# Performance work log

Hardware: AMD Instinct MI355X
Metric: run time of the kernel (lower is better)

## Reference

```python
import jax, jax.numpy as jnp
import numpy as np

B, N, D = 32, 2048, 128
NUM_QUERIES = 16
K_FRAC = 0.5
NUM_SUPPORTS = N - NUM_QUERIES
K_KEEP = int(K_FRAC * NUM_SUPPORTS)  # 1016
M = K_KEEP + NUM_QUERIES             # pooled node count, 1032


def setup_inputs() -> dict:
    key = jax.random.key(0)
    k1, k2, k3 = jax.random.split(key, 3)
    A = jax.random.normal(k1, (B, N, N), dtype=jnp.float32)
    X = jax.random.normal(k2, (B, N, D), dtype=jnp.float32)
    w = jax.random.normal(k3, (D,), dtype=jnp.float32) * 0.1  # proj weight (out_dim=1)
    b = jnp.zeros((1,), dtype=jnp.float32)                     # proj bias
    return {"A": A, "X": X, "w": w, "b": b}


def reference(A, X, w, b):
    # per-node scores: sigmoid(Linear(X)/100), shape [B, N]
    scores = jax.nn.sigmoid((jnp.einsum('bnd,d->bn', X, w) + b[0]) / 100.0)
    support_scores = scores[:, :NUM_SUPPORTS]                     # [B, S]
    intra = support_scores - support_scores.mean(axis=1, keepdims=True)
    # torch.topk(largest=False) == top_k of negated values (ascending order)
    _, support_idx = jax.lax.top_k(-intra, K_KEEP)                # [B, K]
    support_values = jnp.take_along_axis(support_scores, support_idx, axis=1)
    query_idx = jnp.broadcast_to(jnp.arange(NUM_SUPPORTS, N, dtype=support_idx.dtype), (B, NUM_QUERIES))
    query_values = scores[:, NUM_SUPPORTS:]
    idx = jnp.concatenate([support_idx, query_idx], axis=1)       # [B, M]
    values = jnp.concatenate([support_values, query_values], axis=1)  # [B, M]
    # gather + scale node features
    new_X = jnp.take_along_axis(X, idx[:, :, None], axis=1) * values[:, :, None]  # [B, M, D]
    # double gather on adjacency: A[i, idx][:, idx]
    rows = jnp.take_along_axis(A, idx[:, :, None], axis=1)        # [B, M, N]
    new_A = jnp.take_along_axis(rows, idx[:, None, :], axis=2)    # [B, M, M]
    return (new_A, new_X, idx)
```

## Files before the change

### kernel.cpp

```cpp
#include <hip/hip_runtime.h>

#define NB 32
#define NN 2048
#define ND 128
#define NSUP 2032
#define KKEEP 1016
#define MM 1032

typedef unsigned long long u64;
typedef unsigned int u32;

__device__ __forceinline__ float mulrn(float a, float b) {
  float r;
  asm("v_mul_f32 %0, %1, %2" : "=v"(r) : "v"(a), "v"(b));
  return r;
}
__device__ __forceinline__ float addrn(float a, float b) {
  float r;
  asm("v_add_f32 %0, %1, %2" : "=v"(r) : "v"(a), "v"(b));
  return r;
}
__device__ __forceinline__ float fmarn(float a, float b, float c) {
  float r;
  asm("v_fma_f32 %0, %1, %2, %3" : "=v"(r) : "v"(a), "v"(b), "v"(c));
  return r;
}

__global__ __launch_bounds__(256) void k_score(const float* __restrict__ X,
                                               const float* __restrict__ w,
                                               const float* __restrict__ bias,
                                               u64* __restrict__ keys,
                                               float* __restrict__ score) {
#pragma clang fp contract(off)
  int row = blockIdx.x * 256 + threadIdx.x;
  if (row >= NB * NN) return;
  const float* x = X + (size_t)row * ND;

  float l[16];
  #pragma unroll
  for (int k = 0; k < 16; ++k) l[k] = 0.f;
  #pragma unroll
  for (int step = 0; step < 8; ++step) {
    const float* xp = x + step * 16;
    const float* wp = w + step * 16;
    #pragma unroll
    for (int q4 = 0; q4 < 4; ++q4) {
      const float4 xv = *reinterpret_cast<const float4*>(xp + q4 * 4);
      const float4 wv = *reinterpret_cast<const float4*>(wp + q4 * 4);
      l[q4 * 4 + 0] = addrn(mulrn(xv.x, wv.x), l[q4 * 4 + 0]);
      l[q4 * 4 + 1] = addrn(mulrn(xv.y, wv.y), l[q4 * 4 + 1]);
      l[q4 * 4 + 2] = addrn(mulrn(xv.z, wv.z), l[q4 * 4 + 2]);
      l[q4 * 4 + 3] = addrn(mulrn(xv.w, wv.w), l[q4 * 4 + 3]);
    }
  }
  #pragma unroll
  for (int k = 0; k < 8; ++k) l[k] = addrn(l[k], l[k + 8]);
  #pragma unroll
  for (int k = 0; k < 4; ++k) l[k] = addrn(l[k], l[k + 4]);
  l[0] = addrn(l[0], l[2]);
  l[1] = addrn(l[1], l[3]);
  const float dot = addrn(l[0], l[1]);

  const float z = __fdiv_rn(addrn(dot, bias[0]), 100.0f);

  const float xe = -z;
  const float z2 = mulrn(xe, xe);
  float y = fmarn(1.9875691500E-4f, xe, 1.3981999507E-3f);
  y = fmarn(y, xe, 8.3334519073E-3f);
  y = fmarn(y, xe, 4.1665795894E-2f);
  y = fmarn(y, xe, 1.6666665459E-1f);
  y = fmarn(y, xe, 5.0000001201E-1f);
  y = fmarn(y, z2, xe);
  const float e = addrn(y, 1.0f);

  const float s = __fdiv_rn(1.0f, addrn(1.0f, e));

  score[row] = s;

  const u32 sb = __float_as_uint(s);
  const int n = row & (NN - 1);
  keys[row] = ((u64)sb << 32) | (u32)n;
}

__global__ __launch_bounds__(1024) void k_sort(const u64* __restrict__ keys,
                                               const float* __restrict__ score,
                                               int* __restrict__ idxs,
                                               float* __restrict__ vals,
                                               float* __restrict__ out_idx) {
  __shared__ u64 sk[NN];
  int b = blockIdx.x, t = threadIdx.x;
  for (int i = t; i < NN; i += 1024)
    sk[i] = (i < NSUP) ? keys[(size_t)b * NN + i] : ~0ull;
  __syncthreads();
  for (int k = 2; k <= NN; k <<= 1) {
    for (int j = k >> 1; j > 0; j >>= 1) {
      int i = ((t / j) * (j << 1)) + (t % j);
      int p = i + j;
      bool up = ((i & k) == 0);
      u64 ki = sk[i], kp = sk[p];
      if ((ki > kp) == up) { sk[i] = kp; sk[p] = ki; }
      __syncthreads();
    }
  }
  for (int i = t; i < MM; i += 1024) {
    int si = (i < KKEEP) ? (int)(sk[i] & 0xffffffffu) : (NSUP + (i - KKEEP));
    idxs[b * MM + i]    = si;
    vals[b * MM + i]    = score[(size_t)b * NN + si];
    out_idx[b * MM + i] = (float)si;
  }
}

__global__ __launch_bounds__(256) void k_newx(const float* __restrict__ X,
                                              const int* __restrict__ idxs,
                                              const float* __restrict__ vals,
                                              float* __restrict__ out_x) {
  int gid  = blockIdx.x * blockDim.x + threadIdx.x;
  int row  = gid >> 6;
  int lane = threadIdx.x & 63;
  if (row >= NB * MM) return;
  int b  = row / MM;
  int ri = idxs[row];
  float v = vals[row];
  const float2 x2 = *reinterpret_cast<const float2*>(X + ((size_t)b * NN + ri) * ND + lane * 2);
  float2 o = make_float2(x2.x * v, x2.y * v);
  *reinterpret_cast<float2*>(out_x + (size_t)row * ND + lane * 2) = o;
}

__global__ __launch_bounds__(256) void k_newa(const float* __restrict__ A,
                                              const int* __restrict__ idxs,
                                              float* __restrict__ out_a) {
  __shared__ float srow[NN];
  __shared__ int   scols[MM];
  int row = blockIdx.x;
  int b   = row / MM;
  const int* cols = idxs + b * MM;
  for (int i = threadIdx.x; i < MM; i += 256) scols[i] = cols[i];

  int ri = idxs[row];
  const float* arow = A + ((size_t)b * NN + ri) * NN;
  #pragma unroll
  for (int i = 0; i < 2; ++i) {
    int off = (threadIdx.x + i * 256) * 4;
    *reinterpret_cast<float4*>(&srow[off]) =
        *reinterpret_cast<const float4*>(arow + off);
  }
  __syncthreads();

  float4* orow = reinterpret_cast<float4*>(out_a + (size_t)row * MM);
  for (int c = threadIdx.x; c < MM / 4; c += 256) {
    const int4 j4 = *reinterpret_cast<const int4*>(scols + c * 4);
    float4 o;
    o.x = srow[j4.x];
    o.y = srow[j4.y];
    o.z = srow[j4.z];
    o.w = srow[j4.w];
    orow[c] = o;
  }
}

extern "C" void kernel_launch(void* const* d_in, const int* in_sizes, int n_in,
                              void* d_out, int out_size, void* d_ws, size_t ws_size,
                              hipStream_t stream) {
  const float* A    = (const float*)d_in[0];
  const float* X    = (const float*)d_in[1];
  const float* w    = (const float*)d_in[2];
  const float* bias = (const float*)d_in[3];

  float* out0 = (float*)d_out;
  float* out1 = out0 + (size_t)NB * MM * MM;
  float* out2 = out1 + (size_t)NB * MM * ND;

  u64*   keys  = (u64*)d_ws;
  float* score = (float*)(keys + NB * NN);
  int*   idxs  = (int*)(score + NB * NN);
  float* vals  = (float*)(idxs + NB * MM);

  hipLaunchKernelGGL(k_score, dim3(NB * NN / 256), dim3(256), 0, stream, X, w, bias, keys, score);
  hipLaunchKernelGGL(k_sort,  dim3(NB),            dim3(1024), 0, stream, keys, score, idxs, vals, out2);
  hipLaunchKernelGGL(k_newx,  dim3(NB * MM / 4),   dim3(256), 0, stream, X, idxs, vals, out1);
  hipLaunchKernelGGL(k_newa,  dim3(NB * MM),       dim3(256), 0, stream, A, idxs, out0);
}
```

Baseline: 127.3 us.

## Use wave-shuffle bitonic stages in sort and fuse newX into newA kernel

The bitonic sort now does every compare-exchange stage with stride below 64 in registers via wavefront shuffles. Only the wider strides go through shared memory with block barriers, which removes most of the __syncthreads calls and LDS traffic in the single-block-per-batch sort. The separate gather-and-scale kernel for X is folded into the adjacency gather kernel, where 32 threads per row copy and scale one X row, saving a launch. The shuffle network has to reproduce the original bitonic ordering exactly, and the ~0 padding keys stay in place so tie handling is unchanged.

```diff
diff --git a/kernel.cpp b/kernel.cpp
--- a/kernel.cpp
+++ b/kernel.cpp
@@ -82,53 +82,82 @@
   keys[row] = ((u64)sb << 32) | (u32)n;
 }
 
+__device__ __forceinline__ u64 cmpex(u64 v, int j, bool up, int l) {
+  u64 o = __shfl_xor(v, j, 64);
+  bool lower = ((l & j) == 0);
+  u64 mn = (v < o) ? v : o;
+  u64 mx = (v < o) ? o : v;
+  return (lower == up) ? mn : mx;
+}
+
 __global__ __launch_bounds__(1024) void k_sort(const u64* __restrict__ keys,
                                                const float* __restrict__ score,
                                                int* __restrict__ idxs,
                                                float* __restrict__ vals,
                                                float* __restrict__ out_idx) {
   __shared__ u64 sk[NN];
-  int b = blockIdx.x, t = threadIdx.x;
-  for (int i = t; i < NN; i += 1024)
-    sk[i] = (i < NSUP) ? keys[(size_t)b * NN + i] : ~0ull;
+  const int b = blockIdx.x, t = threadIdx.x;
+  const int l = t & 63;
+  const int base0 = (t >> 6) * 128;
+  const size_t bNN = (size_t)b * NN;
+
+  u64 v0 = (base0 + l      < NSUP) ? keys[bNN + base0 + l]      : ~0ull;
+  u64 v1 = (base0 + 64 + l < NSUP) ? keys[bNN + base0 + 64 + l] : ~0ull;
+
+  #pragma unroll
+  for (int k = 2; k <= 32; k <<= 1) {
+    #pragma unroll
+    for (int j = k >> 1; j >= 1; j >>= 1) {
+      bool up = ((l & k) == 0);
+      v0 = cmpex(v0, j, up, l);
+      v1 = cmpex(v1, j, up, l);
+    }
+  }
+  #pragma unroll
+  for (int j = 32; j >= 1; j >>= 1) {
+    v0 = cmpex(v0, j, true, l);
+    v1 = cmpex(v1, j, false, l);
+  }
+  sk[base0 + l]      = v0;
+  sk[base0 + 64 + l] = v1;
   __syncthreads();
-  for (int k = 2; k <= NN; k <<= 1) {
-    for (int j = k >> 1; j > 0; j >>= 1) {
+
+  for (int k = 128; k <= NN; k <<= 1) {
+    for (int j = k >> 1; j >= 64; j >>= 1) {
       int i = ((t / j) * (j << 1)) + (t % j);
       int p = i + j;
       bool up = ((i & k) == 0);
-      u64 ki = sk[i], kp = sk[p];
-      if ((ki > kp) == up) { sk[i] = kp; sk[p] = ki; }
+      u64 a = sk[i], c = sk[p];
+      if ((a > c) == up) { sk[i] = c; sk[p] = a; }
       __syncthreads();
     }
-  }
+    bool up0 = ((base0 & k) == 0);
+    v0 = sk[base0 + l];
+    v1 = sk[base0 + 64 + l];
+    #pragma unroll
+    for (int j = 32; j >= 1; j >>= 1) {
+      v0 = cmpex(v0, j, up0, l);
+      v1 = cmpex(v1, j, up0, l);
+    }
+    sk[base0 + l]      = v0;
+    sk[base0 + 64 + l] = v1;
+    __syncthreads();
+  }
+
   for (int i = t; i < MM; i += 1024) {
     int si = (i < KKEEP) ? (int)(sk[i] & 0xffffffffu) : (NSUP + (i - KKEEP));
     idxs[b * MM + i]    = si;
-    vals[b * MM + i]    = score[(size_t)b * NN + si];
+    vals[b * MM + i]    = score[bNN + si];
     out_idx[b * MM + i] = (float)si;
   }
 }
 
-__global__ __launch_bounds__(256) void k_newx(const float* __restrict__ X,
+__global__ __launch_bounds__(256) void k_newa(const float* __restrict__ A,
+                                              const float* __restrict__ X,
                                               const int* __restrict__ idxs,
                                               const float* __restrict__ vals,
+                                              float* __restrict__ out_a,
                                               float* __restrict__ out_x) {
-  int gid  = blockIdx.x * blockDim.x + threadIdx.x;
-  int row  = gid >> 6;
-  int lane = threadIdx.x & 63;
-  if (row >= NB * MM) return;
-  int b  = row / MM;
-  int ri = idxs[row];
-  float v = vals[row];
-  const float2 x2 = *reinterpret_cast<const float2*>(X + ((size_t)b * NN + ri) * ND + lane * 2);
-  float2 o = make_float2(x2.x * v, x2.y * v);
-  *reinterpret_cast<float2*>(out_x + (size_t)row * ND + lane * 2) = o;
-}
-
-__global__ __launch_bounds__(256) void k_newa(const float* __restrict__ A,
-                                              const int* __restrict__ idxs,
-                                              float* __restrict__ out_a) {
   __shared__ float srow[NN];
   __shared__ int   scols[MM];
   int row = blockIdx.x;
@@ -143,6 +172,14 @@
     int off = (threadIdx.x + i * 256) * 4;
     *reinterpret_cast<float4*>(&srow[off]) =
         *reinterpret_cast<const float4*>(arow + off);
+  }
+
+  if (threadIdx.x < 32) {
+    float v = vals[row];
+    const float4 xv = reinterpret_cast<const float4*>(
+        X + ((size_t)b * NN + ri) * ND)[threadIdx.x];
+    float4 o = make_float4(xv.x * v, xv.y * v, xv.z * v, xv.w * v);
+    reinterpret_cast<float4*>(out_x + (size_t)row * ND)[threadIdx.x] = o;
   }
   __syncthreads();
 
@@ -177,6 +214,5 @@
 
   hipLaunchKernelGGL(k_score, dim3(NB * NN / 256), dim3(256), 0, stream, X, w, bias, keys, score);
   hipLaunchKernelGGL(k_sort,  dim3(NB),            dim3(1024), 0, stream, keys, score, idxs, vals, out2);
-  hipLaunchKernelGGL(k_newx,  dim3(NB * MM / 4),   dim3(256), 0, stream, X, idxs, vals, out1);
-  hipLaunchKernelGGL(k_newa,  dim3(NB * MM),       dim3(256), 0, stream, A, idxs, out0);
-}
+  hipLaunchKernelGGL(k_newa,  dim3(NB * MM),       dim3(256), 0, stream, A, X, idxs, vals, out0, out1);
+}
```

Result: faster. 117.4 us (-7.8%).

## Replace bitonic sort with rank counting and fuse feature gather into adjacency gather

Applied to the files above, without the earlier changes.

The single-block-per-batch bitonic sort is replaced by a counting rank: 8 blocks per batch each rank 254 support keys against all 2032 keys in shared memory and scatter the kept indices to their sorted positions, with extra threads writing the query entries. The separate new_X kernel is folded into the adjacency gather kernel, which now uses 128-thread blocks, vectorized column-index loads, and nontemporal loads and stores for the A rows. This removes one launch, the serial sync-heavy bitonic stages, and lets the sort use more blocks. In exchange it does O(N^2) comparisons per batch and relies on the keys being unique, which the index in the low bits provides.

```diff
diff --git a/kernel.cpp b/kernel.cpp
--- a/kernel.cpp
+++ b/kernel.cpp
@@ -6,9 +6,11 @@
 #define NSUP 2032
 #define KKEEP 1016
 #define MM 1032
+#define SEG 254
 
 typedef unsigned long long u64;
 typedef unsigned int u32;
+typedef float f32x4 __attribute__((ext_vector_type(4)));
 
 __device__ __forceinline__ float mulrn(float a, float b) {
   float r;
@@ -82,79 +84,87 @@
   keys[row] = ((u64)sb << 32) | (u32)n;
 }
 
-__global__ __launch_bounds__(1024) void k_sort(const u64* __restrict__ keys,
-                                               const float* __restrict__ score,
-                                               int* __restrict__ idxs,
-                                               float* __restrict__ vals,
-                                               float* __restrict__ out_idx) {
-  __shared__ u64 sk[NN];
-  int b = blockIdx.x, t = threadIdx.x;
-  for (int i = t; i < NN; i += 1024)
-    sk[i] = (i < NSUP) ? keys[(size_t)b * NN + i] : ~0ull;
+__global__ __launch_bounds__(256) void k_rank(const u64* __restrict__ keys,
+                                              const float* __restrict__ score,
+                                              int* __restrict__ idxs,
+                                              float* __restrict__ vals,
+                                              float* __restrict__ out_idx) {
+  __shared__ u64 lk[NSUP];
+  const int b   = blockIdx.x >> 3;
+  const int seg = blockIdx.x & 7;
+  const int t   = threadIdx.x;
+  const size_t bNN = (size_t)b * NN;
+  const int    bMM = b * MM;
+
+  for (int i = t; i < NSUP; i += 256) lk[i] = keys[bNN + i];
   __syncthreads();
-  for (int k = 2; k <= NN; k <<= 1) {
-    for (int j = k >> 1; j > 0; j >>= 1) {
-      int i = ((t / j) * (j << 1)) + (t % j);
-      int p = i + j;
-      bool up = ((i & k) == 0);
-      u64 ki = sk[i], kp = sk[p];
-      if ((ki > kp) == up) { sk[i] = kp; sk[p] = ki; }
-      __syncthreads();
+
+  if (t < SEG) {
+    const int e  = seg * SEG + t;
+    const u64 my = lk[e];
+    int cnt = 0;
+    #pragma unroll 4
+    for (int s = 0; s < NSUP; s += 4) {
+      const u64 k0 = lk[s], k1 = lk[s + 1], k2 = lk[s + 2], k3 = lk[s + 3];
+      cnt += (int)(k0 < my) + (int)(k1 < my) + (int)(k2 < my) + (int)(k3 < my);
     }
-  }
-  for (int i = t; i < MM; i += 1024) {
-    int si = (i < KKEEP) ? (int)(sk[i] & 0xffffffffu) : (NSUP + (i - KKEEP));
-    idxs[b * MM + i]    = si;
-    vals[b * MM + i]    = score[(size_t)b * NN + si];
-    out_idx[b * MM + i] = (float)si;
+    if (cnt < KKEEP) {
+      idxs[bMM + cnt]    = e;
+      vals[bMM + cnt]    = score[bNN + e];
+      out_idx[bMM + cnt] = (float)e;
+    }
+  } else {
+    const int q   = seg * 2 + (t - SEG);
+    const int e   = NSUP + q;
+    const int pos = KKEEP + q;
+    idxs[bMM + pos]    = e;
+    vals[bMM + pos]    = score[bNN + e];
+    out_idx[bMM + pos] = (float)e;
   }
 }
 
-__global__ __launch_bounds__(256) void k_newx(const float* __restrict__ X,
+__global__ __launch_bounds__(128) void k_newa(const float* __restrict__ A,
+                                              const float* __restrict__ X,
                                               const int* __restrict__ idxs,
                                               const float* __restrict__ vals,
+                                              float* __restrict__ out_a,
                                               float* __restrict__ out_x) {
-  int gid  = blockIdx.x * blockDim.x + threadIdx.x;
-  int row  = gid >> 6;
-  int lane = threadIdx.x & 63;
-  if (row >= NB * MM) return;
-  int b  = row / MM;
-  int ri = idxs[row];
-  float v = vals[row];
-  const float2 x2 = *reinterpret_cast<const float2*>(X + ((size_t)b * NN + ri) * ND + lane * 2);
-  float2 o = make_float2(x2.x * v, x2.y * v);
-  *reinterpret_cast<float2*>(out_x + (size_t)row * ND + lane * 2) = o;
-}
-
-__global__ __launch_bounds__(256) void k_newa(const float* __restrict__ A,
-                                              const int* __restrict__ idxs,
-                                              float* __restrict__ out_a) {
   __shared__ float srow[NN];
   __shared__ int   scols[MM];
   int row = blockIdx.x;
   int b   = row / MM;
   const int* cols = idxs + b * MM;
-  for (int i = threadIdx.x; i < MM; i += 256) scols[i] = cols[i];
+  for (int c = threadIdx.x; c < MM / 4; c += 128)
+    *reinterpret_cast<int4*>(&scols[c * 4]) =
+        reinterpret_cast<const int4*>(cols)[c];
 
   int ri = idxs[row];
   const float* arow = A + ((size_t)b * NN + ri) * NN;
   #pragma unroll
-  for (int i = 0; i < 2; ++i) {
-    int off = (threadIdx.x + i * 256) * 4;
-    *reinterpret_cast<float4*>(&srow[off]) =
-        *reinterpret_cast<const float4*>(arow + off);
+  for (int i = 0; i < 4; ++i) {
+    int off = (threadIdx.x + i * 128) * 4;
+    *reinterpret_cast<f32x4*>(&srow[off]) =
+        __builtin_nontemporal_load(reinterpret_cast<const f32x4*>(arow + off));
+  }
+
+  if (threadIdx.x < 32) {
+    float v = vals[row];
+    const float4 xv = reinterpret_cast<const float4*>(
+        X + ((size_t)b * NN + ri) * ND)[threadIdx.x];
+    float4 o = make_float4(xv.x * v, xv.y * v, xv.z * v, xv.w * v);
+    reinterpret_cast<float4*>(out_x + (size_t)row * ND)[threadIdx.x] = o;
   }
   __syncthreads();
 
-  float4* orow = reinterpret_cast<float4*>(out_a + (size_t)row * MM);
-  for (int c = threadIdx.x; c < MM / 4; c += 256) {
+  f32x4* orow = reinterpret_cast<f32x4*>(out_a + (size_t)row * MM);
+  for (int c = threadIdx.x; c < MM / 4; c += 128) {
     const int4 j4 = *reinterpret_cast<const int4*>(scols + c * 4);
-    float4 o;
+    f32x4 o;
     o.x = srow[j4.x];
     o.y = srow[j4.y];
     o.z = srow[j4.z];
     o.w = srow[j4.w];
-    orow[c] = o;
+    __builtin_nontemporal_store(o, orow + c);
   }
 }
 
@@ -176,7 +186,6 @@
   float* vals  = (float*)(idxs + NB * MM);
 
   hipLaunchKernelGGL(k_score, dim3(NB * NN / 256), dim3(256), 0, stream, X, w, bias, keys, score);
-  hipLaunchKernelGGL(k_sort,  dim3(NB),            dim3(1024), 0, stream, keys, score, idxs, vals, out2);
-  hipLaunchKernelGGL(k_newx,  dim3(NB * MM / 4),   dim3(256), 0, stream, X, idxs, vals, out1);
-  hipLaunchKernelGGL(k_newa,  dim3(NB * MM),       dim3(256), 0, stream, A, idxs, out0);
+  hipLaunchKernelGGL(k_rank,  dim3(NB * 8),        dim3(256), 0, stream, keys, score, idxs, vals, out2);
+  hipLaunchKernelGGL(k_newa,  dim3(NB * MM),       dim3(128), 0, stream, A, X, idxs, vals, out0, out1);
 }
```

Result: faster. 109.8 us (-13.7%).
